# Optimization experiments

Measured on AMD Instinct MI355X. Metric: run time of the kernel, lower is better.

The kernel has to match this reference:

```python
import jax, jax.numpy as jnp
import numpy as np

N_NODES = 100000
N_EDGES = 1600000
D_IN = 128
D_OUT = 128
KEEP_PROB = 0.5  # torch code: p_drop = 1 - self.dropout, dropout=0.5


def setup_inputs() -> dict:
    key = jax.random.key(0)
    k1, k2, k3, k4, k5 = jax.random.split(key, 5)
    x = jax.random.normal(k1, (N_NODES, D_IN), dtype=jnp.float32)
    # Glorot uniform init matching weight_variable_glorot
    init_range = np.sqrt(6.0 / (D_IN + D_OUT))
    W = jax.random.uniform(k2, (D_IN, D_OUT), dtype=jnp.float32,
                           minval=-init_range, maxval=init_range)
    adj_row = jax.random.randint(k3, (N_EDGES,), 0, N_NODES, dtype=jnp.int32)
    adj_col = jax.random.randint(k4, (N_EDGES,), 0, N_NODES, dtype=jnp.int32)
    adj_val = jax.random.uniform(k5, (N_EDGES,), dtype=jnp.float32)
    return {"x": x, "W": W, "adj_row": adj_row, "adj_col": adj_col, "adj_val": adj_val}


def reference(x, W, adj_row, adj_col, adj_val):
    # dropout (always training=True in the torch module), deterministic key
    mask = jax.random.bernoulli(jax.random.key(42), KEEP_PROB, x.shape)
    x = jnp.where(mask, x / KEEP_PROB, 0.0)
    # dense GEMM: [N, D_in] @ [D_in, D_out]
    h = x @ W
    # sparse adjacency SpMM in COO form: out[r] += val * h[c]
    msg = adj_val[:, None] * h[adj_col]            # [E, D_out]
    agg = jax.ops.segment_sum(msg, adj_row, num_segments=N_NODES)
    return jax.nn.relu(agg)
```

## Files before the change

kernel.cpp:

```cpp
#include <hip/hip_runtime.h>
#include <hip/hip_bf16.h>

#define N_NODES 100000
#define N_EDGES 1600000
#define D 128
#define NC 391
#define CCAP 5120
#define NF 3125
#define C1S 32
#define RSS 257
#define GCAP 1024
#define GEMM_H1 1563
#define GEMM_H2 1562

typedef float          floatx4 __attribute__((ext_vector_type(4)));
typedef __bf16         bf16x8  __attribute__((ext_vector_type(8)));
typedef unsigned short ushort8 __attribute__((ext_vector_type(8)));

__device__ __forceinline__ unsigned rotl32(unsigned x, int d) {
    return (x << d) | (x >> (32 - d));
}

__device__ __forceinline__ void threefry_0_42(unsigned c0, unsigned c1,
                                              unsigned& o0, unsigned& o1) {
    const unsigned k0 = 0u, k1 = 42u;
    const unsigned k2 = 0x1BD11BDAu ^ k0 ^ k1;
    unsigned x0 = c0 + k0;
    unsigned x1 = c1 + k1;
#define TF_R4(r0, r1, r2, r3)                      \
    x0 += x1; x1 = rotl32(x1, r0); x1 ^= x0;       \
    x0 += x1; x1 = rotl32(x1, r1); x1 ^= x0;       \
    x0 += x1; x1 = rotl32(x1, r2); x1 ^= x0;       \
    x0 += x1; x1 = rotl32(x1, r3); x1 ^= x0;
    TF_R4(13, 15, 26, 6);  x0 += k1; x1 += k2 + 1u;
    TF_R4(17, 29, 16, 24); x0 += k2; x1 += k0 + 2u;
    TF_R4(13, 15, 26, 6);  x0 += k0; x1 += k1 + 3u;
    TF_R4(17, 29, 16, 24); x0 += k1; x1 += k2 + 4u;
    TF_R4(13, 15, 26, 6);  x0 += k2; x1 += k0 + 5u;
#undef TF_R4
    o0 = x0; o1 = x1;
}

__device__ __forceinline__ bool keep_elem(unsigned i) {
    unsigned o0, o1;
    threefry_0_42(0u, i, o0, o1);
    return (((o0 ^ o1) >> 31) == 0u);
}

__device__ __forceinline__ unsigned short f32_bf16(float f) {
    unsigned u = __float_as_uint(f);
    u += 0x7fffu + ((u >> 16) & 1u);
    return (unsigned short)(u >> 16);
}

__device__ __forceinline__ void gemm_body(const float* __restrict__ x,
                                          const float* __restrict__ W,
                                          unsigned short* __restrict__ hb,
                                          unsigned short (*Wt)[136],
                                          unsigned short (*xs)[136],
                                          int g, int t) {
    {
        int n      = t & 127;
        int k8base = t >> 7;
#pragma unroll
        for (int it = 0; it < 8; ++it) {
            int k8 = (it * 2 + k8base) * 8;
            unsigned short tmp[8];
#pragma unroll
            for (int j = 0; j < 8; ++j)
                tmp[j] = f32_bf16(W[(k8 + j) * 128 + n]);
            *(ushort8*)&Wt[n][k8] = *(ushort8*)tmp;
        }
    }
    {
        int m  = t >> 4;
        int c0 = (t & 15) * 8;
        int r0 = g * 32 + m;
        const float* pa = x + r0 * D + c0;
        const float* pb = x + (r0 + 16) * D + c0;
        float va[8], vb[8];
        *(float4*)&va[0] = ((const float4*)pa)[0];
        *(float4*)&va[4] = ((const float4*)pa)[1];
        *(float4*)&vb[0] = ((const float4*)pb)[0];
        *(float4*)&vb[4] = ((const float4*)pb)[1];
        int ibase = r0 * D + c0;
        unsigned short ta[8], tb[8];
#pragma unroll
        for (int j = 0; j < 8; ++j) {
            float fa = keep_elem((unsigned)(ibase + j))        ? 2.0f * va[j] : 0.0f;
            float fb = keep_elem((unsigned)(ibase + 2048 + j)) ? 2.0f * vb[j] : 0.0f;
            ta[j] = f32_bf16(fa);
            tb[j] = f32_bf16(fb);
        }
        *(ushort8*)&xs[m][c0]      = *(ushort8*)ta;
        *(ushort8*)&xs[16 + m][c0] = *(ushort8*)tb;
    }
    __syncthreads();

    const int w  = t >> 6;
    const int l  = t & 63;
    const int rt = w >> 1;
    const int ctbase = (w & 1) * 4;
    const int mm = l & 15;
    const int q  = l >> 4;
    const int koff = q * 8;
    const unsigned short* xrow = &xs[rt * 16 + mm][0];
    const int growbase = g * 32 + rt * 16;

    for (int ci = 0; ci < 4; ++ci) {
        int ct = ctbase + ci;
        const unsigned short* wrow = &Wt[ct * 16 + mm][0];
        floatx4 acc = {0.f, 0.f, 0.f, 0.f};
#pragma unroll
        for (int kt = 0; kt < 4; ++kt) {
            bf16x8 a = *(const bf16x8*)(xrow + kt * 32 + koff);
            bf16x8 b = *(const bf16x8*)(wrow + kt * 32 + koff);
            acc = __builtin_amdgcn_mfma_f32_16x16x32_bf16(a, b, acc, 0, 0, 0);
        }
        int col = ct * 16 + mm;
#pragma unroll
        for (int reg = 0; reg < 4; ++reg) {
            int grow = growbase + q * 4 + reg;
            hb[grow * D + col] = f32_bf16(acc[reg]);
        }
    }
}

__global__ __launch_bounds__(256)
void k_p1(const float* __restrict__ x, const float* __restrict__ W,
          unsigned short* __restrict__ hb,
          const int* __restrict__ row, const int* __restrict__ col,
          const float* __restrict__ val, int* __restrict__ cnt1,
          int2* __restrict__ buf) {
    __shared__ __align__(16) unsigned short Wt[128][136];
    __shared__ __align__(16) unsigned short xs[32][136];
    __shared__ int h[NC];
    __shared__ int lbase[NC];

    const int t = threadIdx.x;
    if (blockIdx.x >= NC) {
        gemm_body(x, W, hb, Wt, xs, blockIdx.x - NC, t);
        return;
    }

    for (int i = t; i < NC; i += 256) h[i] = 0;
    __syncthreads();

    int rows[16], cols[16];
    float vals[16];
    int base = blockIdx.x * 4096;
#pragma unroll
    for (int k = 0; k < 4; ++k) {
        int e4 = base + (k * 256 + t) * 4;
        if (e4 < N_EDGES) {
            *(int4*)&rows[k * 4]   = *(const int4*)(row + e4);
            *(int4*)&cols[k * 4]   = *(const int4*)(col + e4);
            *(float4*)&vals[k * 4] = *(const float4*)(val + e4);
        } else {
            rows[k * 4] = rows[k * 4 + 1] = rows[k * 4 + 2] = rows[k * 4 + 3] = -1;
        }
    }
#pragma unroll
    for (int j = 0; j < 16; ++j)
        if (rows[j] >= 0) atomicAdd(&h[rows[j] >> 8], 1);
    __syncthreads();

    for (int i = t; i < NC; i += 256) {
        int c = h[i];
        lbase[i] = c ? atomicAdd(&cnt1[i * C1S], c) : 0;
    }
    __syncthreads();
    for (int i = t; i < NC; i += 256) h[i] = 0;
    __syncthreads();

#pragma unroll
    for (int j = 0; j < 16; ++j) {
        if (rows[j] >= 0) {
            int bb  = rows[j] >> 8;
            int pos = lbase[bb] + atomicAdd(&h[bb], 1);
            if (pos < CCAP) {
                int2 ent;
                ent.x = (cols[j] << 7) | ((rows[j] & 255) << 24);
                ent.y = __float_as_int(vals[j]);
                buf[bb * CCAP + pos] = ent;
            }
        }
    }
}

__global__ __launch_bounds__(256)
void k_p2(const float* __restrict__ x, const float* __restrict__ W,
          unsigned short* __restrict__ hb,
          const int* __restrict__ cnt1, int2* __restrict__ buf,
          int* __restrict__ rs) {
    __shared__ __align__(16) unsigned short Wt[128][136];
    __shared__ __align__(16) unsigned short xs[32][136];
    __shared__ int h[4][256];
    __shared__ int wsum[4];

    const int t = threadIdx.x;
    if (blockIdx.x >= NC) {
        gemm_body(x, W, hb, Wt, xs, blockIdx.x - NC + GEMM_H1, t);
        return;
    }

    const int c = blockIdx.x;
    const int w = t >> 6;
    int n = cnt1[c * C1S];
    if (n > CCAP) n = CCAP;
    int2* slab = buf + c * CCAP;

    for (int i = t; i < 1024; i += 256) ((int*)h)[i] = 0;
    __syncthreads();

    int2 er[20];
#pragma unroll
    for (int k = 0; k < 20; ++k) {
        int i = k * 256 + t;
        if (i < n) {
            er[k] = slab[i];
            atomicAdd(&h[w][((unsigned)er[k].x) >> 24], 1);
        }
    }
    __syncthreads();

    int v = h[0][t] + h[1][t] + h[2][t] + h[3][t];
    int xsc = v;
#pragma unroll
    for (int off = 1; off < 64; off <<= 1) {
        int u = __shfl_up(xsc, off);
        if ((t & 63) >= off) xsc += u;
    }
    if ((t & 63) == 63) wsum[t >> 6] = xsc;
    __syncthreads();
    int wo = 0;
    for (int k = 0; k < (t >> 6); ++k) wo += wsum[k];
    int basex = xsc - v + wo;
    rs[c * RSS + t] = basex;
    if (t == 0) rs[c * RSS + 256] = n;
    int s = basex;
#pragma unroll
    for (int wv = 0; wv < 4; ++wv) {
        int tmp = h[wv][t];
        h[wv][t] = s;
        s += tmp;
    }
    __syncthreads();

#pragma unroll
    for (int k = 0; k < 20; ++k) {
        int i = k * 256 + t;
        if (i < n) {
            int pos = atomicAdd(&h[w][((unsigned)er[k].x) >> 24], 1);
            slab[pos] = er[k];
        }
    }
}

__global__ __launch_bounds__(256, 8)
void k_gather(const int* __restrict__ rs, const int2* __restrict__ buf,
              const unsigned short* __restrict__ hb, float* __restrict__ out) {
    __shared__ __align__(16) int2 eL[GCAP];

    const int b = blockIdx.x, t = threadIdx.x;
    const int c = b >> 3;
    const int2* slab = buf + c * CCAP;
    const int* rsb = rs + c * RSS + (b & 7) * 32;
    const int rs0 = rsb[0];
    int nf = rsb[32] - rs0;
    if (nf > GCAP) nf = GCAP;

    for (int i = t; i < nf; i += 256) eL[i] = slab[rs0 + i];
    __syncthreads();

    const int w  = t >> 6;
    const int l2 = (t & 63) * 2;
    const unsigned short* hbl = hb + l2;
    for (int r = 0; r < 8; ++r) {
        int rl = w * 8 + r;
        int s0 = rsb[rl] - rs0;
        int e0 = rsb[rl + 1] - rs0;
        if (e0 > nf) e0 = nf;
        int cc = e0 - s0;
        float a0 = 0.f, a1 = 0.f;
        int i = 0;
        for (; i + 16 <= cc; i += 16) {
            unsigned ex[16];
            float    vv[16];
#pragma unroll
            for (int j = 0; j < 16; ++j) {
                int2 e = eL[s0 + i + j];
                ex[j] = (unsigned)e.x & 0xFFFFFFu;
                vv[j] = __int_as_float(e.y);
            }
            unsigned hv[16];
#pragma unroll
            for (int j = 0; j < 16; ++j)
                hv[j] = *(const unsigned*)(hbl + ex[j]);
#pragma unroll
            for (int j = 0; j < 16; ++j) {
                a0 = fmaf(vv[j], __uint_as_float(hv[j] << 16), a0);
                a1 = fmaf(vv[j], __uint_as_float(hv[j] & 0xffff0000u), a1);
            }
        }
        for (; i + 4 <= cc; i += 4) {
            unsigned ex[4];
            float    vv[4];
#pragma unroll
            for (int j = 0; j < 4; ++j) {
                int2 e = eL[s0 + i + j];
                ex[j] = (unsigned)e.x & 0xFFFFFFu;
                vv[j] = __int_as_float(e.y);
            }
            unsigned hv[4];
#pragma unroll
            for (int j = 0; j < 4; ++j)
                hv[j] = *(const unsigned*)(hbl + ex[j]);
#pragma unroll
            for (int j = 0; j < 4; ++j) {
                a0 = fmaf(vv[j], __uint_as_float(hv[j] << 16), a0);
                a1 = fmaf(vv[j], __uint_as_float(hv[j] & 0xffff0000u), a1);
            }
        }
        for (; i < cc; ++i) {
            int2 e = eL[s0 + i];
            float v = __int_as_float(e.y);
            unsigned hv = *(const unsigned*)(hbl + ((unsigned)e.x & 0xFFFFFFu));
            a0 = fmaf(v, __uint_as_float(hv << 16), a0);
            a1 = fmaf(v, __uint_as_float(hv & 0xffff0000u), a1);
        }
        int grow = (b << 5) + rl;
        float2 rr;
        rr.x = a0 > 0.f ? a0 : 0.f;
        rr.y = a1 > 0.f ? a1 : 0.f;
        *(float2*)(out + grow * D + l2) = rr;
    }
}

extern "C" void kernel_launch(void* const* d_in, const int* in_sizes, int n_in,
                              void* d_out, int out_size, void* d_ws, size_t ws_size,
                              hipStream_t stream) {
    const float* x    = (const float*)d_in[0];
    const float* W    = (const float*)d_in[1];
    const int*   arow = (const int*)d_in[2];
    const int*   acol = (const int*)d_in[3];
    const float* aval = (const float*)d_in[4];
    float* out = (float*)d_out;

    char* ws = (char*)d_ws;
    unsigned short* hb = (unsigned short*)ws;
    size_t off = 25600000;
    int* cnt1 = (int*)(ws + off); off += NC * C1S * 4;
    off = (off + 127) & ~(size_t)127;
    int* rs   = (int*)(ws + off); off += NC * RSS * 4;
    off = (off + 127) & ~(size_t)127;
    int2* buf = (int2*)(ws + off); off += (size_t)NC * CCAP * 8;

    hipMemsetAsync(cnt1, 0, NC * C1S * 4, stream);
    k_p1     <<<NC + GEMM_H1, 256, 0, stream>>>(x, W, hb, arow, acol, aval, cnt1, buf);
    k_p2     <<<NC + GEMM_H2, 256, 0, stream>>>(x, W, hb, cnt1, buf, rs);
    k_gather <<<NF, 256, 0, stream>>>(rs, buf, hb, out);
}
```

Before: 222.5 us.

## Split fused bucket/GEMM kernels, pre-pack W fragments, halve gather block rows

```diff
diff --git a/kernel.cpp b/kernel.cpp
--- a/kernel.cpp
+++ b/kernel.cpp
@@ -6,12 +6,9 @@
 #define D 128
 #define NC 391
 #define CCAP 5120
-#define NF 3125
 #define C1S 32
 #define RSS 257
-#define GCAP 1024
-#define GEMM_H1 1563
-#define GEMM_H2 1562
+#define G2CAP 512
 
 typedef float          floatx4 __attribute__((ext_vector_type(4)));
 typedef __bf16         bf16x8  __attribute__((ext_vector_type(8)));
@@ -53,25 +50,139 @@
     return (unsigned short)(u >> 16);
 }
 
-__device__ __forceinline__ void gemm_body(const float* __restrict__ x,
-                                          const float* __restrict__ W,
-                                          unsigned short* __restrict__ hb,
-                                          unsigned short (*Wt)[136],
-                                          unsigned short (*xs)[136],
-                                          int g, int t) {
-    {
-        int n      = t & 127;
-        int k8base = t >> 7;
-#pragma unroll
-        for (int it = 0; it < 8; ++it) {
-            int k8 = (it * 2 + k8base) * 8;
-            unsigned short tmp[8];
-#pragma unroll
-            for (int j = 0; j < 8; ++j)
-                tmp[j] = f32_bf16(W[(k8 + j) * 128 + n]);
-            *(ushort8*)&Wt[n][k8] = *(ushort8*)tmp;
-        }
-    }
+__global__ __launch_bounds__(256)
+void k_wprep(const float* __restrict__ W, unsigned short* __restrict__ Wf,
+             int* __restrict__ cnt1) {
+    int g = blockIdx.x * 256 + threadIdx.x;
+    for (int i = g; i < NC * C1S; i += 2048) cnt1[i] = 0;
+    int combo = g >> 6, l = g & 63;
+    int ct = combo >> 2, kt = combo & 3;
+    int mm = l & 15, q = l >> 4;
+    unsigned short tmp[8];
+#pragma unroll
+    for (int j = 0; j < 8; ++j)
+        tmp[j] = f32_bf16(W[(kt * 32 + q * 8 + j) * 128 + ct * 16 + mm]);
+    *(ushort8*)&Wf[g * 8] = *(ushort8*)tmp;
+}
+
+__global__ __launch_bounds__(256)
+void k_bucket1(const int* __restrict__ row, const int* __restrict__ col,
+               const float* __restrict__ val, int* __restrict__ cnt1,
+               int2* __restrict__ buf) {
+    __shared__ int h[NC];
+    __shared__ int lbase[NC];
+    const int t = threadIdx.x;
+    for (int i = t; i < NC; i += 256) h[i] = 0;
+    __syncthreads();
+
+    int rows[16], cols[16];
+    float vals[16];
+    int base = blockIdx.x * 4096;
+#pragma unroll
+    for (int k = 0; k < 4; ++k) {
+        int e4 = base + (k * 256 + t) * 4;
+        if (e4 < N_EDGES) {
+            *(int4*)&rows[k * 4]   = *(const int4*)(row + e4);
+            *(int4*)&cols[k * 4]   = *(const int4*)(col + e4);
+            *(float4*)&vals[k * 4] = *(const float4*)(val + e4);
+        } else {
+            rows[k * 4] = rows[k * 4 + 1] = rows[k * 4 + 2] = rows[k * 4 + 3] = -1;
+        }
+    }
+#pragma unroll
+    for (int j = 0; j < 16; ++j)
+        if (rows[j] >= 0) atomicAdd(&h[rows[j] >> 8], 1);
+    __syncthreads();
+
+    for (int i = t; i < NC; i += 256) {
+        int c = h[i];
+        lbase[i] = c ? atomicAdd(&cnt1[i * C1S], c) : 0;
+    }
+    __syncthreads();
+    for (int i = t; i < NC; i += 256) h[i] = 0;
+    __syncthreads();
+
+#pragma unroll
+    for (int j = 0; j < 16; ++j) {
+        if (rows[j] >= 0) {
+            int bb  = rows[j] >> 8;
+            int pos = lbase[bb] + atomicAdd(&h[bb], 1);
+            if (pos < CCAP) {
+                int2 ent;
+                ent.x = (cols[j] << 7) | ((rows[j] & 255) << 24);
+                ent.y = __float_as_int(vals[j]);
+                buf[bb * CCAP + pos] = ent;
+            }
+        }
+    }
+}
+
+__global__ __launch_bounds__(256)
+void k_sort(const int* __restrict__ cnt1, int2* __restrict__ buf,
+            int* __restrict__ rs) {
+    __shared__ int h[4][256];
+    __shared__ int wsum[4];
+
+    const int t = threadIdx.x;
+    const int c = blockIdx.x;
+    const int w = t >> 6;
+    int n = cnt1[c * C1S];
+    if (n > CCAP) n = CCAP;
+    int2* slab = buf + c * CCAP;
+
+    for (int i = t; i < 1024; i += 256) ((int*)h)[i] = 0;
+    __syncthreads();
+
+    int2 er[20];
+#pragma unroll
+    for (int k = 0; k < 20; ++k) {
+        int i = k * 256 + t;
+        if (i < n) {
+            er[k] = slab[i];
+            atomicAdd(&h[w][((unsigned)er[k].x) >> 24], 1);
+        }
+    }
+    __syncthreads();
+
+    int v = h[0][t] + h[1][t] + h[2][t] + h[3][t];
+    int xsc = v;
+#pragma unroll
+    for (int off = 1; off < 64; off <<= 1) {
+        int u = __shfl_up(xsc, off);
+        if ((t & 63) >= off) xsc += u;
+    }
+    if ((t & 63) == 63) wsum[t >> 6] = xsc;
+    __syncthreads();
+    int wo = 0;
+    for (int k = 0; k < (t >> 6); ++k) wo += wsum[k];
+    int basex = xsc - v + wo;
+    rs[c * RSS + t] = basex;
+    if (t == 0) rs[c * RSS + 256] = n;
+    int s = basex;
+#pragma unroll
+    for (int wv = 0; wv < 4; ++wv) {
+        int tmp = h[wv][t];
+        h[wv][t] = s;
+        s += tmp;
+    }
+    __syncthreads();
+
+#pragma unroll
+    for (int k = 0; k < 20; ++k) {
+        int i = k * 256 + t;
+        if (i < n) {
+            int pos = atomicAdd(&h[w][((unsigned)er[k].x) >> 24], 1);
+            slab[pos] = er[k];
+        }
+    }
+}
+
+__global__ __launch_bounds__(256)
+void k_gemm(const float* __restrict__ x, const unsigned short* __restrict__ Wf,
+            unsigned short* __restrict__ hb) {
+    __shared__ __align__(16) unsigned short xs[32][136];
+    const int t = threadIdx.x, g = blockIdx.x;
+
     {
         int m  = t >> 4;
         int c0 = (t & 15) * 8;
@@ -97,26 +208,27 @@
     }
     __syncthreads();
 
-    const int w  = t >> 6;
-    const int l  = t & 63;
-    const int rt = w >> 1;
-    const int ctbase = (w & 1) * 4;
-    const int mm = l & 15;
-    const int q  = l >> 4;
-    const int koff = q * 8;
+    const int w = t >> 6, l = t & 63;
+    const int rt = w >> 1, ctbase = (w & 1) * 4;
+    const int mm = l & 15, q = l >> 4, koff = q * 8;
     const unsigned short* xrow = &xs[rt * 16 + mm][0];
+    bf16x8 af[4];
+#pragma unroll
+    for (int kt = 0; kt < 4; ++kt)
+        af[kt] = *(const bf16x8*)(xrow + kt * 32 + koff);
+
     const int growbase = g * 32 + rt * 16;
-
+#pragma unroll
     for (int ci = 0; ci < 4; ++ci) {
         int ct = ctbase + ci;
-        const unsigned short* wrow = &Wt[ct * 16 + mm][0];
+        bf16x8 wfc[4];
+#pragma unroll
+        for (int kt = 0; kt < 4; ++kt)
+            wfc[kt] = *(const bf16x8*)&Wf[((ct * 4 + kt) * 64 + l) * 8];
         floatx4 acc = {0.f, 0.f, 0.f, 0.f};
 #pragma unroll
-        for (int kt = 0; kt < 4; ++kt) {
-            bf16x8 a = *(const bf16x8*)(xrow + kt * 32 + koff);
-            bf16x8 b = *(const bf16x8*)(wrow + kt * 32 + koff);
-            acc = __builtin_amdgcn_mfma_f32_16x16x32_bf16(a, b, acc, 0, 0, 0);
-        }
+        for (int kt = 0; kt < 4; ++kt)
+            acc = __builtin_amdgcn_mfma_f32_16x16x32_bf16(af[kt], wfc[kt], acc, 0, 0, 0);
         int col = ct * 16 + mm;
 #pragma unroll
         for (int reg = 0; reg < 4; ++reg) {
@@ -126,149 +238,18 @@
     }
 }
 
-__global__ __launch_bounds__(256)
-void k_p1(const float* __restrict__ x, const float* __restrict__ W,
-          unsigned short* __restrict__ hb,
-          const int* __restrict__ row, const int* __restrict__ col,
-          const float* __restrict__ val, int* __restrict__ cnt1,
-          int2* __restrict__ buf) {
-    __shared__ __align__(16) unsigned short Wt[128][136];
-    __shared__ __align__(16) unsigned short xs[32][136];
-    __shared__ int h[NC];
-    __shared__ int lbase[NC];
-
-    const int t = threadIdx.x;
-    if (blockIdx.x >= NC) {
-        gemm_body(x, W, hb, Wt, xs, blockIdx.x - NC, t);
-        return;
-    }
-
-    for (int i = t; i < NC; i += 256) h[i] = 0;
-    __syncthreads();
-
-    int rows[16], cols[16];
-    float vals[16];
-    int base = blockIdx.x * 4096;
-#pragma unroll
-    for (int k = 0; k < 4; ++k) {
-        int e4 = base + (k * 256 + t) * 4;
-        if (e4 < N_EDGES) {
-            *(int4*)&rows[k * 4]   = *(const int4*)(row + e4);
-            *(int4*)&cols[k * 4]   = *(const int4*)(col + e4);
-            *(float4*)&vals[k * 4] = *(const float4*)(val + e4);
-        } else {
-            rows[k * 4] = rows[k * 4 + 1] = rows[k * 4 + 2] = rows[k * 4 + 3] = -1;
-        }
-    }
-#pragma unroll
-    for (int j = 0; j < 16; ++j)
-        if (rows[j] >= 0) atomicAdd(&h[rows[j] >> 8], 1);
-    __syncthreads();
-
-    for (int i = t; i < NC; i += 256) {
-        int c = h[i];
-        lbase[i] = c ? atomicAdd(&cnt1[i * C1S], c) : 0;
-    }
-    __syncthreads();
-    for (int i = t; i < NC; i += 256) h[i] = 0;
-    __syncthreads();
-
-#pragma unroll
-    for (int j = 0; j < 16; ++j) {
-        if (rows[j] >= 0) {
-            int bb  = rows[j] >> 8;
-            int pos = lbase[bb] + atomicAdd(&h[bb], 1);
-            if (pos < CCAP) {
-                int2 ent;
-                ent.x = (cols[j] << 7) | ((rows[j] & 255) << 24);
-                ent.y = __float_as_int(vals[j]);
-                buf[bb * CCAP + pos] = ent;
-            }
-        }
-    }
-}
-
-__global__ __launch_bounds__(256)
-void k_p2(const float* __restrict__ x, const float* __restrict__ W,
-          unsigned short* __restrict__ hb,
-          const int* __restrict__ cnt1, int2* __restrict__ buf,
-          int* __restrict__ rs) {
-    __shared__ __align__(16) unsigned short Wt[128][136];
-    __shared__ __align__(16) unsigned short xs[32][136];
-    __shared__ int h[4][256];
-    __shared__ int wsum[4];
-
-    const int t = threadIdx.x;
-    if (blockIdx.x >= NC) {
-        gemm_body(x, W, hb, Wt, xs, blockIdx.x - NC + GEMM_H1, t);
-        return;
-    }
-
-    const int c = blockIdx.x;
-    const int w = t >> 6;
-    int n = cnt1[c * C1S];
-    if (n > CCAP) n = CCAP;
-    int2* slab = buf + c * CCAP;
-
-    for (int i = t; i < 1024; i += 256) ((int*)h)[i] = 0;
-    __syncthreads();
-
-    int2 er[20];
-#pragma unroll
-    for (int k = 0; k < 20; ++k) {
-        int i = k * 256 + t;
-        if (i < n) {
-            er[k] = slab[i];
-            atomicAdd(&h[w][((unsigned)er[k].x) >> 24], 1);
-        }
-    }
-    __syncthreads();
-
-    int v = h[0][t] + h[1][t] + h[2][t] + h[3][t];
-    int xsc = v;
-#pragma unroll
-    for (int off = 1; off < 64; off <<= 1) {
-        int u = __shfl_up(xsc, off);
-        if ((t & 63) >= off) xsc += u;
-    }
-    if ((t & 63) == 63) wsum[t >> 6] = xsc;
-    __syncthreads();
-    int wo = 0;
-    for (int k = 0; k < (t >> 6); ++k) wo += wsum[k];
-    int basex = xsc - v + wo;
-    rs[c * RSS + t] = basex;
-    if (t == 0) rs[c * RSS + 256] = n;
-    int s = basex;
-#pragma unroll
-    for (int wv = 0; wv < 4; ++wv) {
-        int tmp = h[wv][t];
-        h[wv][t] = s;
-        s += tmp;
-    }
-    __syncthreads();
-
-#pragma unroll
-    for (int k = 0; k < 20; ++k) {
-        int i = k * 256 + t;
-        if (i < n) {
-            int pos = atomicAdd(&h[w][((unsigned)er[k].x) >> 24], 1);
-            slab[pos] = er[k];
-        }
-    }
-}
-
 __global__ __launch_bounds__(256, 8)
 void k_gather(const int* __restrict__ rs, const int2* __restrict__ buf,
               const unsigned short* __restrict__ hb, float* __restrict__ out) {
-    __shared__ __align__(16) int2 eL[GCAP];
-
-    const int b = blockIdx.x, t = threadIdx.x;
-    const int c = b >> 3;
+    __shared__ __align__(16) int2 eL[G2CAP];
+
+    const int B = blockIdx.x, t = threadIdx.x;
+    const int c = B >> 4;
     const int2* slab = buf + c * CCAP;
-    const int* rsb = rs + c * RSS + (b & 7) * 32;
+    const int* rsb = rs + c * RSS + (B & 15) * 16;
     const int rs0 = rsb[0];
-    int nf = rsb[32] - rs0;
-    if (nf > GCAP) nf = GCAP;
+    int nf = rsb[16] - rs0;
+    if (nf > G2CAP) nf = G2CAP;
 
     for (int i = t; i < nf; i += 256) eL[i] = slab[rs0 + i];
     __syncthreads();
@@ -276,11 +257,10 @@
     const int w  = t >> 6;
     const int l2 = (t & 63) * 2;
     const unsigned short* hbl = hb + l2;
-    for (int r = 0; r < 8; ++r) {
-        int rl = w * 8 + r;
-        int s0 = rsb[rl] - rs0;
-        int e0 = rsb[rl + 1] - rs0;
-        if (e0 > nf) e0 = nf;
+    for (int r = 0; r < 4; ++r) {
+        int rl = w * 4 + r;
+        int s0 = rsb[rl] - rs0;     if (s0 > nf) s0 = nf;
+        int e0 = rsb[rl + 1] - rs0; if (e0 > nf) e0 = nf;
         int cc = e0 - s0;
         float a0 = 0.f, a1 = 0.f;
         int i = 0;
@@ -329,11 +309,13 @@
             a0 = fmaf(v, __uint_as_float(hv << 16), a0);
             a1 = fmaf(v, __uint_as_float(hv & 0xffff0000u), a1);
         }
-        int grow = (b << 5) + rl;
-        float2 rr;
-        rr.x = a0 > 0.f ? a0 : 0.f;
-        rr.y = a1 > 0.f ? a1 : 0.f;
-        *(float2*)(out + grow * D + l2) = rr;
+        int grow = (B << 4) + rl;
+        if (grow < N_NODES) {
+            float2 rr;
+            rr.x = a0 > 0.f ? a0 : 0.f;
+            rr.y = a1 > 0.f ? a1 : 0.f;
+            *(float2*)(out + grow * D + l2) = rr;
+        }
     }
 }
 
@@ -352,12 +334,15 @@
     size_t off = 25600000;
     int* cnt1 = (int*)(ws + off); off += NC * C1S * 4;
     off = (off + 127) & ~(size_t)127;
+    unsigned short* Wf = (unsigned short*)(ws + off); off += 32768;
+    off = (off + 127) & ~(size_t)127;
     int* rs   = (int*)(ws + off); off += NC * RSS * 4;
     off = (off + 127) & ~(size_t)127;
     int2* buf = (int2*)(ws + off); off += (size_t)NC * CCAP * 8;
 
-    hipMemsetAsync(cnt1, 0, NC * C1S * 4, stream);
-    k_p1     <<<NC + GEMM_H1, 256, 0, stream>>>(x, W, hb, arow, acol, aval, cnt1, buf);
-    k_p2     <<<NC + GEMM_H2, 256, 0, stream>>>(x, W, hb, cnt1, buf, rs);
-    k_gather <<<NF, 256, 0, stream>>>(rs, buf, hb, out);
-}
+    k_wprep   <<<8, 256, 0, stream>>>(W, Wf, cnt1);
+    k_bucket1 <<<NC, 256, 0, stream>>>(arow, acol, aval, cnt1, buf);
+    k_sort    <<<NC, 256, 0, stream>>>(cnt1, buf, rs);
+    k_gemm    <<<3125, 256, 0, stream>>>(x, Wf, hb);
+    k_gather  <<<NC * 16, 256, 0, stream>>>(rs, buf, hb, out);
+}
```

New measurement: 227.2 us. 2.1% more time.
